# Kernel tuning notes

Measured on AMD Instinct MI355X. Metric: run time of the kernel, lower is better.

The kernel has to match this reference:

```python
import jax, jax.numpy as jnp
import numpy as np

EMBED_DIM = 128
NUM_HEADS = 4
HEAD_DIM = EMBED_DIM // NUM_HEADS


def setup_inputs() -> dict:
    key = jax.random.key(0)
    ks = jax.random.split(key, 12)
    B, N, D = 4, 4096, EMBED_DIM
    s = 1.0 / np.sqrt(D)
    inp = {
        "query": jax.random.normal(ks[0], (B, N, D), dtype=jnp.float32),
        "key": jax.random.normal(ks[1], (B, N, D), dtype=jnp.float32),
        "value": jax.random.normal(ks[2], (B, N, D), dtype=jnp.float32),
        "Wq": jax.random.uniform(ks[3], (D, D), jnp.float32, -s, s),
        "bq": jax.random.uniform(ks[4], (D,), jnp.float32, -s, s),
        "Wk": jax.random.uniform(ks[5], (D, D), jnp.float32, -s, s),
        "bk": jax.random.uniform(ks[6], (D,), jnp.float32, -s, s),
        "Wv": jax.random.uniform(ks[7], (D, D), jnp.float32, -s, s),
        "bv": jax.random.uniform(ks[8], (D,), jnp.float32, -s, s),
        "Wo": jax.random.uniform(ks[9], (D, D), jnp.float32, -s, s),
        "bo": jax.random.uniform(ks[10], (D,), jnp.float32, -s, s),
    }
    return inp


def reference(query, key, value, Wq, bq, Wk, bk, Wv, bv, Wo, bo):
    B, N, D = query.shape
    H, Dh = NUM_HEADS, HEAD_DIM
    scale = Dh ** -0.5
    # Linear projections (torch Linear: x @ W.T + b), split heads -> [B, H, N, Dh]
    Q = (query @ Wq.T + bq).reshape(B, N, H, Dh).transpose(0, 2, 1, 3)
    K = (key @ Wk.T + bk).reshape(B, N, H, Dh).transpose(0, 2, 1, 3)
    V = (value @ Wv.T + bv).reshape(B, N, H, Dh).transpose(0, 2, 1, 3)
    # Attention scores [B, H, N, N]
    scores = jnp.einsum('bhqd,bhkd->bhqk', Q, K) * scale
    attn = jax.nn.softmax(scores, axis=-1)
    ctx = jnp.einsum('bhqk,bhkd->bhqd', attn, V)  # [B, H, N, Dh]
    ctx = ctx.transpose(0, 2, 1, 3).reshape(B, N, D)
    return ctx @ Wo.T + bo
```

## Files before the change

### kernel.cpp

```cpp
#include <hip/hip_runtime.h>
#include <hip/hip_bf16.h>

#define N_SEQ 4096
#define DIM   128
#define NH    4
#define DH    32
#define BATCH 4

#define QSCALE 0.25503495870989204f

typedef __bf16 bf16x8 __attribute__((ext_vector_type(8)));
typedef __bf16 bf16x2 __attribute__((ext_vector_type(2)));
typedef __bf16 bf16x4 __attribute__((ext_vector_type(4)));
typedef float  f32x4  __attribute__((ext_vector_type(4)));

#define MFMA(a, b, c) __builtin_amdgcn_mfma_f32_16x16x32_bf16((a), (b), (c), 0, 0, 0)

static __device__ __forceinline__ bf16x8 cvt8(const float* __restrict__ p) {
    const float4* f4 = reinterpret_cast<const float4*>(p);
    float4 a = f4[0], b = f4[1];
    bf16x8 r;
    r[0] = (__bf16)a.x; r[1] = (__bf16)a.y; r[2] = (__bf16)a.z; r[3] = (__bf16)a.w;
    r[4] = (__bf16)b.x; r[5] = (__bf16)b.y; r[6] = (__bf16)b.z; r[7] = (__bf16)b.w;
    return r;
}

__global__ __launch_bounds__(256) void convert_w(
    const float* __restrict__ Wq, const float* __restrict__ Wk,
    const float* __restrict__ Wv, const float* __restrict__ Wo,
    __bf16* __restrict__ Wb)
{
    const int i = (blockIdx.x * 256 + threadIdx.x) * 4;
    const float* srcs[4] = {Wq, Wk, Wv, Wo};
    #pragma unroll
    for (int w = 0; w < 4; w++) {
        float4 v = *reinterpret_cast<const float4*>(srcs[w] + i);
        bf16x4 o = {(__bf16)v.x, (__bf16)v.y, (__bf16)v.z, (__bf16)v.w};
        *reinterpret_cast<bf16x4*>(Wb + w * (DIM * DIM) + i) = o;
    }
}

__global__ __launch_bounds__(256) void proj_qkv(
    const float* __restrict__ xq, const float* __restrict__ xk, const float* __restrict__ xv,
    const __bf16* __restrict__ Wb,
    const float* __restrict__ bq, const float* __restrict__ bk, const float* __restrict__ bv,
    __bf16* __restrict__ Qs, __bf16* __restrict__ Kb, __bf16* __restrict__ Vt)
{
    const int z = blockIdx.z;
    const float* x    = (z == 0) ? xq : ((z == 1) ? xk : xv);
    const float* bias = (z == 0) ? bq : ((z == 1) ? bk : bv);
    const __bf16* W   = Wb + z * (DIM * DIM);
    const int b    = blockIdx.y;
    const int wave = threadIdx.x >> 6;
    const int lane = threadIdx.x & 63;
    const int quad = lane >> 4, l15 = lane & 15;
    const int n0   = blockIdx.x * 64 + wave * 16;

    bf16x8 a[4];
    const float* xrow = x + (b * N_SEQ + n0 + l15) * DIM + quad * 8;
    a[0] = cvt8(xrow);      a[1] = cvt8(xrow + 32);
    a[2] = cvt8(xrow + 64); a[3] = cvt8(xrow + 96);

    for (int t = 0; t < 8; t++) {
        f32x4 acc = {0.f, 0.f, 0.f, 0.f};
        const __bf16* wrow = W + (t * 16 + l15) * DIM + quad * 8;
        acc = MFMA(a[0], *(const bf16x8*)(wrow),      acc);
        acc = MFMA(a[1], *(const bf16x8*)(wrow + 32), acc);
        acc = MFMA(a[2], *(const bf16x8*)(wrow + 64), acc);
        acc = MFMA(a[3], *(const bf16x8*)(wrow + 96), acc);

        const int d  = t * 16 + l15;
        const int h  = d >> 5, dh = d & 31;
        const float bias_v = bias[d];
        if (z == 0) {
            __bf16* dst = Qs + ((b * NH + h) * N_SEQ) * DH + dh;
            #pragma unroll
            for (int r = 0; r < 4; r++) {
                const int n = n0 + quad * 4 + r;
                dst[n * DH] = (__bf16)((acc[r] + bias_v) * QSCALE);
            }
        } else if (z == 1) {
            __bf16* dst = Kb + ((b * NH + h) * N_SEQ) * DH + dh;
            #pragma unroll
            for (int r = 0; r < 4; r++) {
                const int n = n0 + quad * 4 + r;
                const int np = (n & ~63) | (((n & 3) << 4) | ((n & 63) >> 2));
                dst[np * DH] = (__bf16)(acc[r] + bias_v);
            }
        } else {
            __bf16* dst = Vt + ((b * NH + h) * DH + dh) * N_SEQ;
            #pragma unroll
            for (int r = 0; r < 4; r++) {
                const int n = n0 + quad * 4 + r;
                dst[n] = (__bf16)(acc[r] + bias_v);
            }
        }
    }
}

__global__ __launch_bounds__(256, 2) void flash_attn(
    const __bf16* __restrict__ Qs, const __bf16* __restrict__ Kb,
    const __bf16* __restrict__ Vt, __bf16* __restrict__ ctxb)
{
    __shared__ __align__(16) char smem[37888];
    char* const Kbase = smem;
    char* const Vbase = smem + 10240;
    char* const Pbase = smem + 19456;

    const int bid  = blockIdx.x;
    const int bh   = bid & 15;
    const int qc   = bid >> 4;
    const int tid  = threadIdx.x;
    const int wave = tid >> 6, lane = tid & 63;
    const int quad = lane >> 4, l15 = lane & 15;
    const int n0   = qc * 128 + wave * 32;

    const __bf16* Qp = Qs + (bh * N_SEQ + n0) * DH;
    bf16x8 qf0 = *(const bf16x8*)(Qp + l15 * DH + quad * 8);
    bf16x8 qf1 = *(const bf16x8*)(Qp + (16 + l15) * DH + quad * 8);

    const __bf16* gK = Kb + (size_t)bh * N_SEQ * DH + tid * 8;
    const __bf16* gV = Vt + ((size_t)bh * DH + (tid >> 3)) * N_SEQ + (tid & 7) * 8;
    const int kofsK = (tid >> 2) * 80 + (tid & 3) * 16;
    const int kofsV = (tid >> 3) * 144 + (tid & 7) * 16;

    {
        bf16x8 kr = *(const bf16x8*)(gK);
        bf16x8 vr = *(const bf16x8*)(gV);
        *(bf16x8*)(Kbase + kofsK) = kr;
        *(bf16x8*)(Vbase + kofsV) = vr;
    }
    __syncthreads();

    f32x4 c00 = {0.f,0.f,0.f,0.f}, c01 = {0.f,0.f,0.f,0.f};
    f32x4 c10 = {0.f,0.f,0.f,0.f}, c11 = {0.f,0.f,0.f,0.f};
    float l0[4] = {0.f,0.f,0.f,0.f}, l1[4] = {0.f,0.f,0.f,0.f};
    char* const Pw = Pbase + wave * 4608;
    const f32x4 z4 = {0.f,0.f,0.f,0.f};

    for (int kb = 0; kb < N_SEQ / 64; kb++) {
        const int cur = kb & 1;
        const char* Kc = Kbase + cur * 5120;
        const char* Vc = Vbase + cur * 4608;

        const int kn = (kb + 1) & (N_SEQ / 64 - 1);
        bf16x8 krn = *(const bf16x8*)(gK + kn * 64 * DH);
        bf16x8 vrn = *(const bf16x8*)(gV + kn * 64);

        bf16x8 kf0 = *(const bf16x8*)(Kc + l15 * 80 + quad * 16);
        bf16x8 kf1 = *(const bf16x8*)(Kc + (16 + l15) * 80 + quad * 16);
        bf16x8 kf2 = *(const bf16x8*)(Kc + (32 + l15) * 80 + quad * 16);
        bf16x8 kf3 = *(const bf16x8*)(Kc + (48 + l15) * 80 + quad * 16);

        f32x4 s00 = MFMA(qf0, kf0, z4), s01 = MFMA(qf0, kf1, z4);
        f32x4 s02 = MFMA(qf0, kf2, z4), s03 = MFMA(qf0, kf3, z4);
        f32x4 s10 = MFMA(qf1, kf0, z4), s11 = MFMA(qf1, kf1, z4);
        f32x4 s12 = MFMA(qf1, kf2, z4), s13 = MFMA(qf1, kf3, z4);

        #pragma unroll
        for (int r = 0; r < 4; r++) {
            float p0 = __builtin_amdgcn_exp2f(s00[r]);
            float p1 = __builtin_amdgcn_exp2f(s01[r]);
            float p2 = __builtin_amdgcn_exp2f(s02[r]);
            float p3 = __builtin_amdgcn_exp2f(s03[r]);
            l0[r] += (p0 + p1) + (p2 + p3);
            bf16x4 pk = {(__bf16)p0, (__bf16)p1, (__bf16)p2, (__bf16)p3};
            *(bf16x4*)(Pw + (quad * 4 + r) * 144 + l15 * 8) = pk;
        }
        #pragma unroll
        for (int r = 0; r < 4; r++) {
            float p0 = __builtin_amdgcn_exp2f(s10[r]);
            float p1 = __builtin_amdgcn_exp2f(s11[r]);
            float p2 = __builtin_amdgcn_exp2f(s12[r]);
            float p3 = __builtin_amdgcn_exp2f(s13[r]);
            l1[r] += (p0 + p1) + (p2 + p3);
            bf16x4 pk = {(__bf16)p0, (__bf16)p1, (__bf16)p2, (__bf16)p3};
            *(bf16x4*)(Pw + (16 + quad * 4 + r) * 144 + l15 * 8) = pk;
        }

        bf16x8 pf00 = *(const bf16x8*)(Pw + l15 * 144 + quad * 16);
        bf16x8 pf01 = *(const bf16x8*)(Pw + l15 * 144 + 64 + quad * 16);
        bf16x8 pf10 = *(const bf16x8*)(Pw + (16 + l15) * 144 + quad * 16);
        bf16x8 pf11 = *(const bf16x8*)(Pw + (16 + l15) * 144 + 64 + quad * 16);
        bf16x8 vf00 = *(const bf16x8*)(Vc + l15 * 144 + quad * 16);
        bf16x8 vf01 = *(const bf16x8*)(Vc + (16 + l15) * 144 + quad * 16);
        bf16x8 vf10 = *(const bf16x8*)(Vc + l15 * 144 + 64 + quad * 16);
        bf16x8 vf11 = *(const bf16x8*)(Vc + (16 + l15) * 144 + 64 + quad * 16);

        c00 = MFMA(pf00, vf00, c00); c01 = MFMA(pf00, vf01, c01);
        c00 = MFMA(pf01, vf10, c00); c01 = MFMA(pf01, vf11, c01);
        c10 = MFMA(pf10, vf00, c10); c11 = MFMA(pf10, vf01, c11);
        c10 = MFMA(pf11, vf10, c10); c11 = MFMA(pf11, vf11, c11);

        *(bf16x8*)(Kbase + (cur ^ 1) * 5120 + kofsK) = krn;
        *(bf16x8*)(Vbase + (cur ^ 1) * 4608 + kofsV) = vrn;
        __syncthreads();
    }

    const int b = bh >> 2, h = bh & 3;
    #pragma unroll
    for (int r = 0; r < 4; r++) {
        float ls = l0[r];
        ls += __shfl_xor(ls, 1); ls += __shfl_xor(ls, 2);
        ls += __shfl_xor(ls, 4); ls += __shfl_xor(ls, 8);
        const float inv = 1.0f / ls;
        const int n = n0 + quad * 4 + r;
        __bf16* dst = ctxb + (b * N_SEQ + n) * DIM + h * DH;
        dst[l15]      = (__bf16)(c00[r] * inv);
        dst[16 + l15] = (__bf16)(c01[r] * inv);
    }
    #pragma unroll
    for (int r = 0; r < 4; r++) {
        float ls = l1[r];
        ls += __shfl_xor(ls, 1); ls += __shfl_xor(ls, 2);
        ls += __shfl_xor(ls, 4); ls += __shfl_xor(ls, 8);
        const float inv = 1.0f / ls;
        const int n = n0 + 16 + quad * 4 + r;
        __bf16* dst = ctxb + (b * N_SEQ + n) * DIM + h * DH;
        dst[l15]      = (__bf16)(c10[r] * inv);
        dst[16 + l15] = (__bf16)(c11[r] * inv);
    }
}

__global__ __launch_bounds__(256) void out_proj(
    const __bf16* __restrict__ ctxb, const __bf16* __restrict__ WoB,
    const float* __restrict__ bo, float* __restrict__ out)
{
    const int b    = blockIdx.y;
    const int wave = threadIdx.x >> 6, lane = threadIdx.x & 63;
    const int quad = lane >> 4, l15 = lane & 15;
    const int n0   = blockIdx.x * 64 + wave * 16;

    bf16x8 a[4];
    const __bf16* crow = ctxb + (b * N_SEQ + n0 + l15) * DIM + quad * 8;
    a[0] = *(const bf16x8*)(crow);
    a[1] = *(const bf16x8*)(crow + 32);
    a[2] = *(const bf16x8*)(crow + 64);
    a[3] = *(const bf16x8*)(crow + 96);

    for (int t = 0; t < 8; t++) {
        f32x4 acc = {0.f, 0.f, 0.f, 0.f};
        const __bf16* wrow = WoB + (t * 16 + l15) * DIM + quad * 8;
        acc = MFMA(a[0], *(const bf16x8*)(wrow),      acc);
        acc = MFMA(a[1], *(const bf16x8*)(wrow + 32), acc);
        acc = MFMA(a[2], *(const bf16x8*)(wrow + 64), acc);
        acc = MFMA(a[3], *(const bf16x8*)(wrow + 96), acc);

        const int d = t * 16 + l15;
        const float bias_v = bo[d];
        #pragma unroll
        for (int r = 0; r < 4; r++) {
            const int n = n0 + quad * 4 + r;
            out[(b * N_SEQ + n) * DIM + d] = acc[r] + bias_v;
        }
    }
}

extern "C" void kernel_launch(void* const* d_in, const int* in_sizes, int n_in,
                              void* d_out, int out_size, void* d_ws, size_t ws_size,
                              hipStream_t stream)
{
    const float* query = (const float*)d_in[0];
    const float* key   = (const float*)d_in[1];
    const float* value = (const float*)d_in[2];
    const float* Wq = (const float*)d_in[3];
    const float* bq = (const float*)d_in[4];
    const float* Wk = (const float*)d_in[5];
    const float* bk = (const float*)d_in[6];
    const float* Wv = (const float*)d_in[7];
    const float* bv = (const float*)d_in[8];
    const float* Wo = (const float*)d_in[9];
    const float* bo = (const float*)d_in[10];
    float* out = (float*)d_out;

    char* ws = (char*)d_ws;
    const size_t e = (size_t)BATCH * N_SEQ * DIM;
    __bf16* Qs   = (__bf16*)(ws);
    __bf16* Kb   = (__bf16*)(ws + 2 * e);
    __bf16* Vt   = (__bf16*)(ws + 4 * e);
    __bf16* ctxb = (__bf16*)(ws + 6 * e);
    __bf16* Wb   = (__bf16*)(ws + 8 * e);

    convert_w<<<dim3(16), 256, 0, stream>>>(Wq, Wk, Wv, Wo, Wb);
    proj_qkv<<<dim3(64, BATCH, 3), 256, 0, stream>>>(
        query, key, value, Wb, bq, bk, bv, Qs, Kb, Vt);
    flash_attn<<<dim3(512), 256, 0, stream>>>(Qs, Kb, Vt, ctxb);
    out_proj<<<dim3(64, BATCH), 256, 0, stream>>>(ctxb, Wb + 3 * DIM * DIM, bo, out);
}
```

Before: 178.1 us.

## Halve flash-attention query tile per wave and swap operands for V projection stores

New measurement: 181.8 us. +2.1%, slower.

```diff
diff --git a/kernel.cpp b/kernel.cpp
--- a/kernel.cpp
+++ b/kernel.cpp
@@ -64,45 +64,58 @@
     for (int t = 0; t < 8; t++) {
         f32x4 acc = {0.f, 0.f, 0.f, 0.f};
         const __bf16* wrow = W + (t * 16 + l15) * DIM + quad * 8;
-        acc = MFMA(a[0], *(const bf16x8*)(wrow),      acc);
-        acc = MFMA(a[1], *(const bf16x8*)(wrow + 32), acc);
-        acc = MFMA(a[2], *(const bf16x8*)(wrow + 64), acc);
-        acc = MFMA(a[3], *(const bf16x8*)(wrow + 96), acc);
-
-        const int d  = t * 16 + l15;
-        const int h  = d >> 5, dh = d & 31;
-        const float bias_v = bias[d];
-        if (z == 0) {
-            __bf16* dst = Qs + ((b * NH + h) * N_SEQ) * DH + dh;
+        bf16x8 w0 = *(const bf16x8*)(wrow);
+        bf16x8 w1 = *(const bf16x8*)(wrow + 32);
+        bf16x8 w2 = *(const bf16x8*)(wrow + 64);
+        bf16x8 w3 = *(const bf16x8*)(wrow + 96);
+
+        if (z != 2) {
+            acc = MFMA(a[0], w0, acc);
+            acc = MFMA(a[1], w1, acc);
+            acc = MFMA(a[2], w2, acc);
+            acc = MFMA(a[3], w3, acc);
+
+            const int d  = t * 16 + l15;
+            const int h  = d >> 5, dh = d & 31;
+            const float bias_v = bias[d];
+            if (z == 0) {
+                __bf16* dst = Qs + ((b * NH + h) * N_SEQ) * DH + dh;
+                #pragma unroll
+                for (int r = 0; r < 4; r++) {
+                    const int n = n0 + quad * 4 + r;
+                    dst[n * DH] = (__bf16)((acc[r] + bias_v) * QSCALE);
+                }
+            } else {
+                __bf16* dst = Kb + ((b * NH + h) * N_SEQ) * DH + dh;
+                #pragma unroll
+                for (int r = 0; r < 4; r++) {
+                    const int n = n0 + quad * 4 + r;
+                    const int np = (n & ~63) | (((n & 3) << 4) | ((n & 63) >> 2));
+                    dst[np * DH] = (__bf16)(acc[r] + bias_v);
+                }
+            }
+        } else {
+            acc = MFMA(w0, a[0], acc);
+            acc = MFMA(w1, a[1], acc);
+            acc = MFMA(w2, a[2], acc);
+            acc = MFMA(w3, a[3], acc);
+
+            const int n = n0 + l15;
             #pragma unroll
             for (int r = 0; r < 4; r++) {
-                const int n = n0 + quad * 4 + r;
-                dst[n * DH] = (__bf16)((acc[r] + bias_v) * QSCALE);
-            }
-        } else if (z == 1) {
-            __bf16* dst = Kb + ((b * NH + h) * N_SEQ) * DH + dh;
-            #pragma unroll
-            for (int r = 0; r < 4; r++) {
-                const int n = n0 + quad * 4 + r;
-                const int np = (n & ~63) | (((n & 3) << 4) | ((n & 63) >> 2));
-                dst[np * DH] = (__bf16)(acc[r] + bias_v);
-            }
-        } else {
-            __bf16* dst = Vt + ((b * NH + h) * DH + dh) * N_SEQ;
-            #pragma unroll
-            for (int r = 0; r < 4; r++) {
-                const int n = n0 + quad * 4 + r;
-                dst[n] = (__bf16)(acc[r] + bias_v);
+                const int d = t * 16 + quad * 4 + r;
+                const int h = d >> 5, dh = d & 31;
+                Vt[((b * NH + h) * DH + dh) * N_SEQ + n] = (__bf16)(acc[r] + bias[d]);
             }
         }
     }
 }
 
-__global__ __launch_bounds__(256, 2) void flash_attn(
+__global__ __launch_bounds__(256, 4) void flash_attn(
     const __bf16* __restrict__ Qs, const __bf16* __restrict__ Kb,
     const __bf16* __restrict__ Vt, __bf16* __restrict__ ctxb)
 {
-    __shared__ __align__(16) char smem[37888];
+    __shared__ __align__(16) char smem[28672];
     char* const Kbase = smem;
     char* const Vbase = smem + 10240;
     char* const Pbase = smem + 19456;
@@ -113,11 +126,10 @@
     const int tid  = threadIdx.x;
     const int wave = tid >> 6, lane = tid & 63;
     const int quad = lane >> 4, l15 = lane & 15;
-    const int n0   = qc * 128 + wave * 32;
+    const int n0   = qc * 64 + wave * 16;
 
     const __bf16* Qp = Qs + (bh * N_SEQ + n0) * DH;
-    bf16x8 qf0 = *(const bf16x8*)(Qp + l15 * DH + quad * 8);
-    bf16x8 qf1 = *(const bf16x8*)(Qp + (16 + l15) * DH + quad * 8);
+    bf16x8 qf = *(const bf16x8*)(Qp + l15 * DH + quad * 8);
 
     const __bf16* gK = Kb + (size_t)bh * N_SEQ * DH + tid * 8;
     const __bf16* gV = Vt + ((size_t)bh * DH + (tid >> 3)) * N_SEQ + (tid & 7) * 8;
@@ -132,10 +144,9 @@
     }
     __syncthreads();
 
-    f32x4 c00 = {0.f,0.f,0.f,0.f}, c01 = {0.f,0.f,0.f,0.f};
-    f32x4 c10 = {0.f,0.f,0.f,0.f}, c11 = {0.f,0.f,0.f,0.f};
-    float l0[4] = {0.f,0.f,0.f,0.f}, l1[4] = {0.f,0.f,0.f,0.f};
-    char* const Pw = Pbase + wave * 4608;
+    f32x4 c0 = {0.f,0.f,0.f,0.f}, c1 = {0.f,0.f,0.f,0.f};
+    float l0[4] = {0.f,0.f,0.f,0.f};
+    char* const Pw = Pbase + wave * 2304;
     const f32x4 z4 = {0.f,0.f,0.f,0.f};
 
     for (int kb = 0; kb < N_SEQ / 64; kb++) {
@@ -152,45 +163,29 @@
         bf16x8 kf2 = *(const bf16x8*)(Kc + (32 + l15) * 80 + quad * 16);
         bf16x8 kf3 = *(const bf16x8*)(Kc + (48 + l15) * 80 + quad * 16);
 
-        f32x4 s00 = MFMA(qf0, kf0, z4), s01 = MFMA(qf0, kf1, z4);
-        f32x4 s02 = MFMA(qf0, kf2, z4), s03 = MFMA(qf0, kf3, z4);
-        f32x4 s10 = MFMA(qf1, kf0, z4), s11 = MFMA(qf1, kf1, z4);
-        f32x4 s12 = MFMA(qf1, kf2, z4), s13 = MFMA(qf1, kf3, z4);
+        f32x4 s0 = MFMA(qf, kf0, z4), s1 = MFMA(qf, kf1, z4);
+        f32x4 s2 = MFMA(qf, kf2, z4), s3 = MFMA(qf, kf3, z4);
 
         #pragma unroll
         for (int r = 0; r < 4; r++) {
-            float p0 = __builtin_amdgcn_exp2f(s00[r]);
-            float p1 = __builtin_amdgcn_exp2f(s01[r]);
-            float p2 = __builtin_amdgcn_exp2f(s02[r]);
-            float p3 = __builtin_amdgcn_exp2f(s03[r]);
+            float p0 = __builtin_amdgcn_exp2f(s0[r]);
+            float p1 = __builtin_amdgcn_exp2f(s1[r]);
+            float p2 = __builtin_amdgcn_exp2f(s2[r]);
+            float p3 = __builtin_amdgcn_exp2f(s3[r]);
             l0[r] += (p0 + p1) + (p2 + p3);
             bf16x4 pk = {(__bf16)p0, (__bf16)p1, (__bf16)p2, (__bf16)p3};
             *(bf16x4*)(Pw + (quad * 4 + r) * 144 + l15 * 8) = pk;
         }
-        #pragma unroll
-        for (int r = 0; r < 4; r++) {
-            float p0 = __builtin_amdgcn_exp2f(s10[r]);
-            float p1 = __builtin_amdgcn_exp2f(s11[r]);
-            float p2 = __builtin_amdgcn_exp2f(s12[r]);
-            float p3 = __builtin_amdgcn_exp2f(s13[r]);
-            l1[r] += (p0 + p1) + (p2 + p3);
-            bf16x4 pk = {(__bf16)p0, (__bf16)p1, (__bf16)p2, (__bf16)p3};
-            *(bf16x4*)(Pw + (16 + quad * 4 + r) * 144 + l15 * 8) = pk;
-        }
-
-        bf16x8 pf00 = *(const bf16x8*)(Pw + l15 * 144 + quad * 16);
-        bf16x8 pf01 = *(const bf16x8*)(Pw + l15 * 144 + 64 + quad * 16);
-        bf16x8 pf10 = *(const bf16x8*)(Pw + (16 + l15) * 144 + quad * 16);
-        bf16x8 pf11 = *(const bf16x8*)(Pw + (16 + l15) * 144 + 64 + quad * 16);
+
+        bf16x8 pf0 = *(const bf16x8*)(Pw + l15 * 144 + quad * 16);
+        bf16x8 pf1 = *(const bf16x8*)(Pw + l15 * 144 + 64 + quad * 16);
         bf16x8 vf00 = *(const bf16x8*)(Vc + l15 * 144 + quad * 16);
         bf16x8 vf01 = *(const bf16x8*)(Vc + (16 + l15) * 144 + quad * 16);
         bf16x8 vf10 = *(const bf16x8*)(Vc + l15 * 144 + 64 + quad * 16);
         bf16x8 vf11 = *(const bf16x8*)(Vc + (16 + l15) * 144 + 64 + quad * 16);
 
-        c00 = MFMA(pf00, vf00, c00); c01 = MFMA(pf00, vf01, c01);
-        c00 = MFMA(pf01, vf10, c00); c01 = MFMA(pf01, vf11, c01);
-        c10 = MFMA(pf10, vf00, c10); c11 = MFMA(pf10, vf01, c11);
-        c10 = MFMA(pf11, vf10, c10); c11 = MFMA(pf11, vf11, c11);
+        c0 = MFMA(pf0, vf00, c0); c1 = MFMA(pf0, vf01, c1);
+        c0 = MFMA(pf1, vf10, c0); c1 = MFMA(pf1, vf11, c1);
 
         *(bf16x8*)(Kbase + (cur ^ 1) * 5120 + kofsK) = krn;
         *(bf16x8*)(Vbase + (cur ^ 1) * 4608 + kofsV) = vrn;
@@ -206,19 +201,8 @@
         const float inv = 1.0f / ls;
         const int n = n0 + quad * 4 + r;
         __bf16* dst = ctxb + (b * N_SEQ + n) * DIM + h * DH;
-        dst[l15]      = (__bf16)(c00[r] * inv);
-        dst[16 + l15] = (__bf16)(c01[r] * inv);
-    }
-    #pragma unroll
-    for (int r = 0; r < 4; r++) {
-        float ls = l1[r];
-        ls += __shfl_xor(ls, 1); ls += __shfl_xor(ls, 2);
-        ls += __shfl_xor(ls, 4); ls += __shfl_xor(ls, 8);
-        const float inv = 1.0f / ls;
-        const int n = n0 + 16 + quad * 4 + r;
-        __bf16* dst = ctxb + (b * N_SEQ + n) * DIM + h * DH;
-        dst[l15]      = (__bf16)(c10[r] * inv);
-        dst[16 + l15] = (__bf16)(c11[r] * inv);
+        dst[l15]      = (__bf16)(c0[r] * inv);
+        dst[16 + l15] = (__bf16)(c1[r] * inv);
     }
 }
 
@@ -284,6 +268,6 @@
     convert_w<<<dim3(16), 256, 0, stream>>>(Wq, Wk, Wv, Wo, Wb);
     proj_qkv<<<dim3(64, BATCH, 3), 256, 0, stream>>>(
         query, key, value, Wb, bq, bk, bv, Qs, Kb, Vt);
-    flash_attn<<<dim3(512), 256, 0, stream>>>(Qs, Kb, Vt, ctxb);
+    flash_attn<<<dim3(1024), 256, 0, stream>>>(Qs, Kb, Vt, ctxb);
     out_proj<<<dim3(64, BATCH), 256, 0, stream>>>(ctxb, Wb + 3 * DIM * DIM, bo, out);
 }
```
